# Kernel tuning notes

Measured on AMD Instinct MI355X. Metric: run time of the kernel, lower is better.

The kernel has to match this reference:

```python
import jax, jax.numpy as jnp
import numpy as np

N_NODES = 30000
N_EDGES = 480000
C = 32          # channel multiplicity of hidden irreps (32x0e + 32x1o)
L = 3           # graph_net_steps
H = 64          # radial MLP hidden width
NB = 8          # num radial basis functions
NS = 5          # num_species
R_MAX = 4.0
AVG_NEIGH = 16.0
N_PATHS = 5     # tensor-product paths per layer


def setup_inputs() -> dict:
    key = jax.random.key(0)
    ks = jax.random.split(key, 16)

    def w(k, shape, fan_in):
        return jax.random.normal(k, shape, jnp.float32) / np.sqrt(fan_in)

    return {
        "vectors": jax.random.normal(ks[0], (N_EDGES, 3), jnp.float32),
        "node_specie": jax.random.randint(ks[1], (N_NODES,), 0, NS),
        "senders": jax.random.randint(ks[2], (N_EDGES,), 0, N_NODES),
        "receivers": jax.random.randint(ks[3], (N_EDGES,), 0, N_NODES),
        "emb": jax.random.normal(ks[4], (NS, C), jnp.float32),
        "w_rad1": w(ks[5], (L, NB, H), NB),
        "w_rad2": w(ks[6], (L, H, H), H),
        "w_rad_out": w(ks[7], (L, H, N_PATHS * C), H),
        "w_lin_s": w(ks[8], (L, 2 * C, 2 * C), 2 * C),
        "w_lin_v": w(ks[9], (L, 3 * C, C), 3 * C),
        "w_sc_s": w(ks[10], (L, NS, C, 2 * C), C),
        "w_sc_v": w(ks[11], (L, NS, C, C), C),
        "w_out1": w(ks[12], (C, 16), C),
        "w_out2": w(ks[13], (16, 1), 16),
    }


def _envelope(x, p=6):
    # smooth polynomial cutoff, = 1 at x=0, = 0 (with zero derivs) at x=1
    u = (1.0 - (p + 1) * (p + 2) / 2 * x**p + p * (p + 2) * x**(p + 1)
         - p * (p + 1) / 2 * x**(p + 2))
    return jnp.where(x < 1.0, u, 0.0)


def _radial_basis(lengths):
    # bessel radial basis [E, NB] with smooth cutoff envelope
    n = jnp.arange(1, NB + 1, dtype=jnp.float32)
    x = lengths / R_MAX
    b = np.sqrt(2.0 / R_MAX) * jnp.sin(n * np.pi * x[:, None]) \
        / jnp.maximum(lengths, 1e-9)[:, None]
    return b * _envelope(x)[:, None]


def reference(vectors, node_specie, senders, receivers, emb, w_rad1, w_rad2,
              w_rad_out, w_lin_s, w_lin_v, w_sc_s, w_sc_v, w_out1, w_out2):
    vectors = vectors / R_MAX                       # as in original __call__
    lengths = jnp.linalg.norm(vectors, axis=-1)
    nhat = vectors / jnp.maximum(lengths, 1e-9)[:, None]   # unit edge vectors
    rb = _radial_basis(lengths)                     # [E, NB]

    s = emb[node_specie]                            # [N, C] scalars (0e)
    v = jnp.zeros((s.shape[0], C, 3), s.dtype)      # [N, C, 3] vectors (1o)

    for l in range(L):
        # radial MLP -> per-path, per-channel edge weights
        h = jax.nn.silu(rb @ w_rad1[l])
        h = jax.nn.silu(h @ w_rad2[l])
        wgt = (h @ w_rad_out[l]).reshape(-1, N_PATHS, C)        # [E, 5, C]

        s_u = s[senders]                                         # [E, C]
        v_u = v[senders]                                         # [E, C, 3]
        ndv = jnp.einsum('ed,ecd->ec', nhat, v_u)                # <n, v>

        # CG tensor-product message paths with spherical harmonics of n
        p0 = wgt[:, 0] * s_u                                     # 0e x Y0 -> 0e
        p1 = wgt[:, 1] * ndv                                     # 1o x Y1 -> 0e
        p2 = wgt[:, 2][:, :, None] * (s_u[:, :, None] * nhat[:, None, :])  # 0e x Y1 -> 1o
        p3 = wgt[:, 3][:, :, None] * v_u                         # 1o x Y0 -> 1o
        p4 = wgt[:, 4][:, :, None] * (nhat[:, None, :] * ndv[:, :, None] - v_u / 3.0)  # 1o x Y2 -> 1o

        agg_s = jax.ops.segment_sum(jnp.concatenate([p0, p1], 1), receivers,
                                    num_segments=N_NODES) / AVG_NEIGH      # [N, 2C]
        agg_v = jax.ops.segment_sum(jnp.concatenate([p2, p3, p4], 1), receivers,
                                    num_segments=N_NODES) / AVG_NEIGH      # [N, 3C, 3]

        sg = agg_s @ w_lin_s[l]                                  # [N, 2C]: C feats + C gates
        vn = jnp.einsum('npd,pc->ncd', agg_v, w_lin_v[l])        # [N, C, 3]
        # self-connection: per-species linear (== tp with species one-hot)
        sg = sg + jnp.einsum('nc,nck->nk', s, w_sc_s[l][node_specie])
        vn = vn + jnp.einsum('ncd,nck->nkd', v, w_sc_v[l][node_specie])

        s_new, gates = jnp.split(sg, 2, axis=1)
        s = jax.nn.silu(s_new)                                   # even activation
        v = jax.nn.silu(gates)[:, :, None] * vn                  # gated 1o

    e = (s @ w_out1) @ w_out2            # Linear '16x0e' -> Linear '0e'
    return e[:, 0]                        # per-node energy [N]
```

## Files before the change

### kernel.cpp

```cpp
#include <hip/hip_runtime.h>
#include <math.h>

#define NNODES 30000
#define NEDGES 480000
#define NC 32
#define NL 3
#define NH 64
#define NBASIS 8
#define NSPEC 5
#define INV_AVG 0.0625f

typedef _Float16 half2v __attribute__((ext_vector_type(2)));
typedef _Float16 half4v __attribute__((ext_vector_type(4)));
typedef _Float16 half8v __attribute__((ext_vector_type(8)));
typedef float    float4v __attribute__((ext_vector_type(4)));
typedef unsigned int uint32;

__device__ __forceinline__ float silu_f(float x) {
    return x / (1.f + __expf(-x));
}
__device__ __forceinline__ float rdlane(float v, int k) {
    return __uint_as_float(__builtin_amdgcn_readlane(__float_as_uint(v), k));
}


__global__ void count_kernel(const int* __restrict__ receivers, int* __restrict__ deg) {
    int e = blockIdx.x * blockDim.x + threadIdx.x;
    if (e >= NEDGES) return;
    atomicAdd(&deg[receivers[e]], 1);
}

__global__ void scan_kernel(const int* __restrict__ deg, int* __restrict__ rowstart) {
    __shared__ int lsum[256];
    __shared__ int loff[256];
    int t = threadIdx.x;
    int lo = t * 118;
    int hi = min(lo + 118, NNODES);
    int s = 0;
    for (int i = lo; i < hi; ++i) s += deg[i];
    lsum[t] = s;
    __syncthreads();
    if (t == 0) {
        int run = 0;
        for (int i = 0; i < 256; ++i) { loff[i] = run; run += lsum[i]; }
    }
    __syncthreads();
    int run = loff[t];
    for (int i = lo; i < hi; ++i) { rowstart[i] = run; run += deg[i]; }
    if (t == 0) rowstart[NNODES] = NEDGES;
}

__global__ void copy_cursor_kernel(const int* __restrict__ rowstart, int* __restrict__ cursor) {
    int i = blockIdx.x * blockDim.x + threadIdx.x;
    if (i < NNODES) cursor[i] = rowstart[i];
}

__global__ void fill_kernel(const int* __restrict__ receivers,
                            int* __restrict__ cursor, int* __restrict__ epos) {
    int e = blockIdx.x * blockDim.x + threadIdx.x;
    if (e >= NEDGES) return;
    epos[e] = atomicAdd(&cursor[receivers[e]], 1);
}

__global__ void geom_perm_kernel(const float* __restrict__ vec,
                                 const int* __restrict__ senders,
                                 const int* __restrict__ epos,
                                 float* __restrict__ nh_perm,
                                 int* __restrict__ snd_perm,
                                 float* __restrict__ rb_perm) {
    int e = blockIdx.x * blockDim.x + threadIdx.x;
    if (e >= NEDGES) return;
    float vx = vec[3*e+0] * 0.25f;
    float vy = vec[3*e+1] * 0.25f;
    float vz = vec[3*e+2] * 0.25f;
    float len = sqrtf(vx*vx + vy*vy + vz*vz);
    float inv = 1.f / fmaxf(len, 1e-9f);
    int p = epos[e];
    *(float4*)(nh_perm + (size_t)p*4) = make_float4(vx*inv, vy*inv, vz*inv, 0.f);
    snd_perm[p] = senders[e];
    float x = len * 0.25f;
    float x3 = x*x*x;
    float x6 = x3*x3;
    float x7 = x6*x;
    float x8 = x7*x;
    float env = (x < 1.f) ? (1.f - 28.f*x6 + 48.f*x7 - 21.f*x8) : 0.f;
    float scale = 0.7071067811865476f * inv * env;
    float rbv[8];
    #pragma unroll
    for (int i = 0; i < NBASIS; ++i)
        rbv[i] = scale * sinf((float)(i+1) * 3.14159265358979f * x);
    *(float4*)(rb_perm + (size_t)p*8)     = make_float4(rbv[0], rbv[1], rbv[2], rbv[3]);
    *(float4*)(rb_perm + (size_t)p*8 + 4) = make_float4(rbv[4], rbv[5], rbv[6], rbv[7]);
}

__global__ void prepw_kernel(const float* __restrict__ w1, const float* __restrict__ w2,
                             const float* __restrict__ w3,
                             float* __restrict__ w1t, _Float16* __restrict__ w2f,
                             _Float16* __restrict__ w3f) {
    int t = blockIdx.x * blockDim.x + threadIdx.x;
    if (t < NL * 64 * 8) {
        int l = t / 512, r = t % 512, k = r >> 3, b = r & 7;
        w1t[t] = w1[l * 512 + b * 64 + k];
    }
    int u = t - NL * 64 * 8;
    if (u >= 0 && u < NL * 2 * 4 * 64 * 8) {
        int e = u & 7, lane = (u >> 3) & 63, nt = (u >> 9) & 3, ks = (u >> 11) & 1, l = u >> 12;
        int k = ks * 32 + ((lane >> 4) << 3) + e;
        int col = nt * 16 + (lane & 15);
        w2f[u] = (_Float16)w2[l * 4096 + k * 64 + col];
    }
    int v = t - NL * 64 * 8 - NL * 2 * 4 * 64 * 8;
    if (v >= 0 && v < NL * 2 * 10 * 64 * 8) {
        int q = v / 5120, rem = v % 5120;
        int l = q >> 1, ks = q & 1;
        int nt = rem >> 9, lane = (rem >> 3) & 63, e = rem & 7;
        int k = ks * 32 + ((lane >> 4) << 3) + e;
        int col = nt * 16 + (lane & 15);
        w3f[v] = (_Float16)w3[l * 10240 + k * 160 + col];
    }
}

__global__ void init_kernel(const int* __restrict__ specie,
                            const float* __restrict__ emb,
                            _Float16* __restrict__ s) {
    int t = blockIdx.x * blockDim.x + threadIdx.x;
    if (t >= NNODES * NC) return;
    int n = t >> 5;
    int c = t & 31;
    s[t] = (_Float16)emb[specie[n] * NC + c];
}

__global__ __launch_bounds__(256) void mlpm_kernel(
    const float* __restrict__ rb_perm,
    const float* __restrict__ w1t,
    const _Float16* __restrict__ w2f,
    const _Float16* __restrict__ w3f,
    _Float16* __restrict__ wgt16)
{
    __shared__ float w1lds[512];
    __shared__ _Float16 tile[4][16][72];

    for (int t = threadIdx.x; t < 512; t += 256) w1lds[t] = w1t[t];
    __syncthreads();

    int lane = threadIdx.x & 63;
    int wid  = threadIdx.x >> 6;
    int c16 = lane & 15;
    int kg  = lane >> 4;
    int ibase = blockIdx.x * 64 + wid * 16;
    int g = blockIdx.x * 4 + wid;

    float4 ra4 = *(const float4*)(rb_perm + (size_t)(ibase + c16) * 8);
    float4 rb4 = *(const float4*)(rb_perm + (size_t)(ibase + c16) * 8 + 4);

    half8v a0, a1;
    #pragma unroll
    for (int e = 0; e < 8; ++e) {
        const float* wr0 = w1lds + (kg * 8 + e) * 8;
        float d0;
        d0 = ra4.x * wr0[0];
        d0 = fmaf(ra4.y, wr0[1], d0);
        d0 = fmaf(ra4.z, wr0[2], d0);
        d0 = fmaf(ra4.w, wr0[3], d0);
        d0 = fmaf(rb4.x, wr0[4], d0);
        d0 = fmaf(rb4.y, wr0[5], d0);
        d0 = fmaf(rb4.z, wr0[6], d0);
        d0 = fmaf(rb4.w, wr0[7], d0);
        a0[e] = (_Float16)silu_f(d0);
        const float* wr1 = w1lds + (32 + kg * 8 + e) * 8;
        float d1;
        d1 = ra4.x * wr1[0];
        d1 = fmaf(ra4.y, wr1[1], d1);
        d1 = fmaf(ra4.z, wr1[2], d1);
        d1 = fmaf(ra4.w, wr1[3], d1);
        d1 = fmaf(rb4.x, wr1[4], d1);
        d1 = fmaf(rb4.y, wr1[5], d1);
        d1 = fmaf(rb4.z, wr1[6], d1);
        d1 = fmaf(rb4.w, wr1[7], d1);
        a1[e] = (_Float16)silu_f(d1);
    }

    _Float16* tw = &tile[wid][0][0];
    float4v zero4 = {0.f, 0.f, 0.f, 0.f};
    #pragma unroll
    for (int nt = 0; nt < 4; ++nt) {
        half8v b0 = *(const half8v*)(w2f + (size_t)(nt) * 512 + lane * 8);
        half8v b1 = *(const half8v*)(w2f + (size_t)(4 + nt) * 512 + lane * 8);
        float4v acc = __builtin_amdgcn_mfma_f32_16x16x32_f16(a0, b0, zero4, 0, 0, 0);
        acc = __builtin_amdgcn_mfma_f32_16x16x32_f16(a1, b1, acc, 0, 0, 0);
        #pragma unroll
        for (int r = 0; r < 4; ++r)
            tw[(kg * 4 + r) * 72 + nt * 16 + c16] = (_Float16)silu_f(acc[r]);
    }

    half8v a2 = *(const half8v*)(tw + c16 * 72 + kg * 8);
    half8v a3 = *(const half8v*)(tw + c16 * 72 + 32 + kg * 8);

    _Float16* out = wgt16 + (size_t)g * 2560 + lane * 4;
    #pragma unroll
    for (int nt = 0; nt < 10; ++nt) {
        half8v b0 = *(const half8v*)(w3f + (size_t)(nt) * 512 + lane * 8);
        half8v b1 = *(const half8v*)(w3f + (size_t)(10 + nt) * 512 + lane * 8);
        float4v acc = __builtin_amdgcn_mfma_f32_16x16x32_f16(a2, b0, zero4, 0, 0, 0);
        acc = __builtin_amdgcn_mfma_f32_16x16x32_f16(a3, b1, acc, 0, 0, 0);
        half4v o;
        o[0] = (_Float16)acc[0];
        o[1] = (_Float16)acc[1];
        o[2] = (_Float16)acc[2];
        o[3] = (_Float16)acc[3];
        *(half4v*)(out + nt * 256) = o;
    }
}

__global__ __launch_bounds__(512) void gather_tp_kernel(
    const _Float16* __restrict__ wgt16,
    const float* __restrict__ nh_perm,
    const int* __restrict__ snd_perm,
    const int* __restrict__ rowstart, const int* __restrict__ deg,
    const _Float16* __restrict__ s_in, const _Float16* __restrict__ v_in,
    float* __restrict__ agg_s,
    float* __restrict__ agg_v)
{
    int lane = threadIdx.x & 63;
    int wid  = threadIdx.x >> 6;
    int n = blockIdx.x * 8 + wid;
    if (n >= NNODES) return;

    int c = lane & 31;
    int half = lane >> 5;

    int c16g = c & 15;
    int off0 = (2 * half + (c >> 4)) * 256 + c16g * 4;
    int off1 = (4 + 2 * half + (c >> 4)) * 256 + c16g * 4;
    int off2 = (8 + (c >> 4)) * 256 + c16g * 4;

    float accS = 0.f;
    float aVa0 = 0.f, aVa1 = 0.f, aVa2 = 0.f;
    float aVb0 = 0.f, aVb1 = 0.f, aVb2 = 0.f;

    int start = rowstart[n];
    int cnt   = deg[n];

    int snd_n = 0;
    float4 nh_n = make_float4(0.f, 0.f, 0.f, 0.f);
    if (cnt > 0) {
        snd_n = snd_perm[start];
        nh_n  = *(const float4*)(nh_perm + (size_t)start * 4);
    }

    for (int i = 0; i < cnt; ++i) {
        int idx = start + i;
        int snd = snd_n;
        float4 nh = nh_n;
        size_t base_e = (size_t)(idx >> 4) * 2560 + ((idx & 15) >> 2) * 64 + (idx & 3);

        float d0  = (float)wgt16[base_e + off0];
        float d1  = (float)wgt16[base_e + off1];
        float d2f = (float)wgt16[base_e + off2];

        if (i + 1 < cnt) {
            snd_n = snd_perm[idx + 1];
            nh_n  = *(const float4*)(nh_perm + (size_t)(idx + 1) * 4);
        }

        float su = (float)s_in[(size_t)snd * NC + c];
        float v0 = (float)v_in[(size_t)snd * 96 + c];
        float v1 = (float)v_in[(size_t)snd * 96 + 32 + c];
        float v2 = (float)v_in[(size_t)snd * 96 + 64 + c];
        float ndv = nh.x * v0;
        ndv = fmaf(nh.y, v1, ndv);
        ndv = fmaf(nh.z, v2, ndv);

        float sSel = half ? ndv : su;
        accS = fmaf(d0, sSel, accS);
        float scale = half ? d1 : d1 * su;
        float f0 = half ? v0 : nh.x;
        float f1 = half ? v1 : nh.y;
        float f2 = half ? v2 : nh.z;
        aVa0 = fmaf(scale, f0, aVa0);
        aVa1 = fmaf(scale, f1, aVa1);
        aVa2 = fmaf(scale, f2, aVa2);
        float m4 = half ? 0.f : d2f;
        aVb0 = fmaf(m4, fmaf(nh.x, ndv, -v0 * (1.f / 3.f)), aVb0);
        aVb1 = fmaf(m4, fmaf(nh.y, ndv, -v1 * (1.f / 3.f)), aVb1);
        aVb2 = fmaf(m4, fmaf(nh.z, ndv, -v2 * (1.f / 3.f)), aVb2);
    }

    agg_s[(size_t)n * 64 + lane] = accS;
    float* av = agg_v + (size_t)n * 288;
    if (half == 0) {
        av[c * 3 + 0] = aVa0; av[c * 3 + 1] = aVa1; av[c * 3 + 2] = aVa2;
        av[(64 + c) * 3 + 0] = aVb0; av[(64 + c) * 3 + 1] = aVb1; av[(64 + c) * 3 + 2] = aVb2;
    } else {
        av[(32 + c) * 3 + 0] = aVa0; av[(32 + c) * 3 + 1] = aVa1; av[(32 + c) * 3 + 2] = aVa2;
    }
}

__global__ __launch_bounds__(256) void node_kernel(
    const int* __restrict__ specie,
    const float* __restrict__ agg_s, const float* __restrict__ agg_v,
    const _Float16* __restrict__ s_in,  const _Float16* __restrict__ v_in,
    const float* __restrict__ wls,
    const float* __restrict__ wlv,
    const float* __restrict__ wscs,
    const float* __restrict__ wscv,
    _Float16* __restrict__ s_out, _Float16* __restrict__ v_out)
{
    __shared__ float sAV[4][288];
    __shared__ float sVO[4][96];

    int lane = threadIdx.x & 63;
    int wid  = threadIdx.x >> 6;
    int n = blockIdx.x * 4 + wid;
    if (n >= NNODES) return;
    int sp = specie[n];

    const float* av = agg_v + (size_t)n * 288;
    sAV[wid][lane]       = av[lane];
    sAV[wid][64 + lane]  = av[64 + lane];
    sAV[wid][128 + lane] = av[128 + lane];
    sAV[wid][192 + lane] = av[192 + lane];
    if (lane < 32) sAV[wid][256 + lane] = av[256 + lane];
    const _Float16* vo = v_in + (size_t)n * 96;
    if (lane < 32) {
        sVO[wid][lane]      = (float)vo[lane];
        sVO[wid][32 + lane] = (float)vo[32 + lane];
        sVO[wid][64 + lane] = (float)vo[64 + lane];
    }

    float asv = agg_s[(size_t)n * 64 + lane];
    float sv  = (float)s_in[(size_t)n * 32 + (lane & 31)];

    __syncthreads();

    float sg = 0.f;
    #pragma unroll
    for (int j = 0; j < 64; ++j)
        sg = fmaf(rdlane(asv, j), wls[j * 64 + lane], sg);
    sg *= INV_AVG;
    const float* ws = wscs + (size_t)sp * 32 * 64;
    #pragma unroll
    for (int j = 0; j < 32; ++j)
        sg = fmaf(rdlane(sv, j), ws[j * 64 + lane], sg);
    float act  = silu_f(sg);
    float gate = __shfl(act, (lane & 31) + 32);

    int c = lane & 31;
    int h = lane >> 5;
    float vn1 = 0.f, vn2 = 0.f;
    #pragma unroll
    for (int p = 0; p < 96; ++p) {
        float w = wlv[p * 32 + c];
        vn1 = fmaf(sAV[wid][3 * p + h], w, vn1);
        vn2 = fmaf(sAV[wid][3 * p + 2], w, vn2);
    }
    vn1 *= INV_AVG; vn2 *= INV_AVG;
    const float* wv = wscv + (size_t)sp * 32 * 32;
    #pragma unroll
    for (int j = 0; j < 32; ++j) {
        float w = wv[j * 32 + c];
        vn1 = fmaf(sVO[wid][h * 32 + j], w, vn1);
        vn2 = fmaf(sVO[wid][64 + j],     w, vn2);
    }

    if (lane < 32) s_out[(size_t)n * 32 + lane] = (_Float16)act;
    v_out[(size_t)n * 96 + h * 32 + c] = (_Float16)(gate * vn1);
    if (h == 0) v_out[(size_t)n * 96 + 64 + c] = (_Float16)(gate * vn2);
}

__global__ void out_kernel(const _Float16* __restrict__ s,
                           const float* __restrict__ w1,
                           const float* __restrict__ w2,
                           float* __restrict__ out) {
    int n = blockIdx.x * blockDim.x + threadIdx.x;
    if (n >= NNODES) return;
    float sv[NC];
    #pragma unroll
    for (int c = 0; c < NC; ++c) sv[c] = (float)s[(size_t)n * NC + c];
    float e = 0.f;
    #pragma unroll
    for (int j = 0; j < 16; ++j) {
        float tj = 0.f;
        #pragma unroll
        for (int c = 0; c < NC; ++c) tj += sv[c] * w1[c * 16 + j];
        e += tj * w2[j];
    }
    out[n] = e;
}

extern "C" void kernel_launch(void* const* d_in, const int* in_sizes, int n_in,
                              void* d_out, int out_size, void* d_ws, size_t ws_size,
                              hipStream_t stream) {
    const float* vectors   = (const float*)d_in[0];
    const int*   specie    = (const int*)  d_in[1];
    const int*   senders   = (const int*)  d_in[2];
    const int*   receivers = (const int*)  d_in[3];
    const float* emb       = (const float*)d_in[4];
    const float* w_rad1    = (const float*)d_in[5];
    const float* w_rad2    = (const float*)d_in[6];
    const float* w_rad_out = (const float*)d_in[7];
    const float* w_lin_s   = (const float*)d_in[8];
    const float* w_lin_v   = (const float*)d_in[9];
    const float* w_sc_s    = (const float*)d_in[10];
    const float* w_sc_v    = (const float*)d_in[11];
    const float* w_out1    = (const float*)d_in[12];
    const float* w_out2    = (const float*)d_in[13];

    char* base = (char*)d_ws;
    size_t off = 0;
    auto alloc = [&](size_t bytes) { char* q = base + off; off += (bytes + 255) & ~(size_t)255; return q; };

    float*    nh_perm  = (float*)alloc((size_t)NEDGES * 4 * 4);
    float*    rb_perm  = (float*)alloc((size_t)NEDGES * 8 * 4);
    int*      snd_perm = (int*)alloc((size_t)NEDGES * 4);
    int*      epos     = (int*)alloc((size_t)NEDGES * 4);
    _Float16* s_a      = (_Float16*)alloc((size_t)NNODES * NC * 2);
    _Float16* v_a      = (_Float16*)alloc((size_t)NNODES * NC * 3 * 2);
    _Float16* s_b      = (_Float16*)alloc((size_t)NNODES * NC * 2);
    _Float16* v_b      = (_Float16*)alloc((size_t)NNODES * NC * 3 * 2);
    float*    aggs     = (float*)alloc((size_t)NNODES * 2 * NC * 4);
    float*    aggv     = (float*)alloc((size_t)NNODES * 3 * NC * 3 * 4);
    int* deg        = (int*)alloc((size_t)NNODES * 4);
    int* rowstart   = (int*)alloc((size_t)(NNODES + 4) * 4);
    int* cursor     = (int*)alloc((size_t)NNODES * 4);
    float*    w1t      = (float*)alloc((size_t)NL * 64 * 8 * 4);
    _Float16* w2f      = (_Float16*)alloc((size_t)NL * 2 * 4 * 64 * 8 * 2);
    _Float16* w3f      = (_Float16*)alloc((size_t)NL * 2 * 10 * 64 * 8 * 2);
    _Float16* wgt16    = (_Float16*)alloc((size_t)NEDGES * 160 * 2);
    if (off > ws_size) return;

    (void)hipMemsetAsync(deg, 0, NNODES * sizeof(int), stream);
    count_kernel<<<(NEDGES + 255) / 256, 256, 0, stream>>>(receivers, deg);
    scan_kernel<<<1, 256, 0, stream>>>(deg, rowstart);
    copy_cursor_kernel<<<(NNODES + 255) / 256, 256, 0, stream>>>(rowstart, cursor);
    fill_kernel<<<(NEDGES + 255) / 256, 256, 0, stream>>>(receivers, cursor, epos);
    geom_perm_kernel<<<(NEDGES + 255) / 256, 256, 0, stream>>>(
        vectors, senders, epos, nh_perm, snd_perm, rb_perm);
    int prep_n = NL * 64 * 8 + NL * 2 * 4 * 64 * 8 + NL * 2 * 10 * 64 * 8;
    prepw_kernel<<<(prep_n + 255) / 256, 256, 0, stream>>>(
        w_rad1, w_rad2, w_rad_out, w1t, w2f, w3f);

    init_kernel<<<(NNODES * NC + 255) / 256, 256, 0, stream>>>(specie, emb, s_a);
    (void)hipMemsetAsync(v_a, 0, (size_t)NNODES * NC * 3 * 2, stream);

    _Float16* si = s_a; _Float16* vi = v_a; _Float16* so = s_b; _Float16* vo = v_b;
    for (int l = 0; l < NL; ++l) {
        mlpm_kernel<<<NEDGES / 64, 256, 0, stream>>>(
            rb_perm,
            w1t + (size_t)l * 512,
            w2f + (size_t)l * 4096,
            w3f + (size_t)l * 10240,
            wgt16);
        gather_tp_kernel<<<(NNODES + 7) / 8, 512, 0, stream>>>(
            wgt16, nh_perm, snd_perm, rowstart, deg, si, vi, aggs, aggv);
        node_kernel<<<(NNODES + 3) / 4, 256, 0, stream>>>(
            specie, aggs, aggv, si, vi,
            w_lin_s + (size_t)l * 64 * 64,
            w_lin_v + (size_t)l * 96 * 32,
            w_sc_s + (size_t)l * NSPEC * NC * 64,
            w_sc_v + (size_t)l * NSPEC * NC * NC,
            so, vo);
        _Float16* ts = si; si = so; so = ts;
        _Float16* tv = vi; vi = vo; vo = tv;
    }

    out_kernel<<<(NNODES + 255) / 256, 256, 0, stream>>>(si, w_out1, w_out2, (float*)d_out);
}
```

Baseline: 751.2 us.

## Store radial MLP weights edge-major so gather reads contiguous per-edge rows

```diff
diff --git a/kernel.cpp b/kernel.cpp
--- a/kernel.cpp
+++ b/kernel.cpp
@@ -21,6 +21,9 @@
 }
 __device__ __forceinline__ float rdlane(float v, int k) {
     return __uint_as_float(__builtin_amdgcn_readlane(__float_as_uint(v), k));
+}
+__device__ __forceinline__ half2v u2h(uint32 u) {
+    union { uint32 u; half2v h; } x; x.u = u; return x.h;
 }
 
 
@@ -138,7 +141,7 @@
     _Float16* __restrict__ wgt16)
 {
     __shared__ float w1lds[512];
-    __shared__ _Float16 tile[4][16][72];
+    __shared__ __align__(16) _Float16 lds2[4][2688];
 
     for (int t = threadIdx.x; t < 512; t += 256) w1lds[t] = w1t[t];
     __syncthreads();
@@ -180,7 +183,7 @@
         a1[e] = (_Float16)silu_f(d1);
     }
 
-    _Float16* tw = &tile[wid][0][0];
+    _Float16* tw = &lds2[wid][0];
     float4v zero4 = {0.f, 0.f, 0.f, 0.f};
     #pragma unroll
     for (int nt = 0; nt < 4; ++nt) {
@@ -196,19 +199,29 @@
     half8v a2 = *(const half8v*)(tw + c16 * 72 + kg * 8);
     half8v a3 = *(const half8v*)(tw + c16 * 72 + 32 + kg * 8);
 
-    _Float16* out = wgt16 + (size_t)g * 2560 + lane * 4;
     #pragma unroll
     for (int nt = 0; nt < 10; ++nt) {
         half8v b0 = *(const half8v*)(w3f + (size_t)(nt) * 512 + lane * 8);
         half8v b1 = *(const half8v*)(w3f + (size_t)(10 + nt) * 512 + lane * 8);
         float4v acc = __builtin_amdgcn_mfma_f32_16x16x32_f16(a2, b0, zero4, 0, 0, 0);
         acc = __builtin_amdgcn_mfma_f32_16x16x32_f16(a3, b1, acc, 0, 0, 0);
-        half4v o;
-        o[0] = (_Float16)acc[0];
-        o[1] = (_Float16)acc[1];
-        o[2] = (_Float16)acc[2];
-        o[3] = (_Float16)acc[3];
-        *(half4v*)(out + nt * 256) = o;
+        int slot;
+        if (nt < 4)      slot = nt * 32 + 2 * c16;
+        else if (nt < 8) slot = (nt - 4) * 32 + 2 * c16 + 1;
+        else             slot = 128 + (nt - 8) * 16 + c16;
+        #pragma unroll
+        for (int r = 0; r < 4; ++r)
+            tw[(kg * 4 + r) * 168 + slot] = (_Float16)acc[r];
+    }
+
+    _Float16* gout = wgt16 + (size_t)g * 2560;
+    #pragma unroll
+    for (int u = 0; u < 5; ++u) {
+        int g4 = u * 64 + lane;
+        int edge = g4 / 20;
+        int part = g4 % 20;
+        half8v vv = *(const half8v*)(tw + edge * 168 + part * 8);
+        *(half8v*)(gout + edge * 160 + part * 8) = vv;
     }
 }
 
@@ -229,11 +242,6 @@
     int c = lane & 31;
     int half = lane >> 5;
 
-    int c16g = c & 15;
-    int off0 = (2 * half + (c >> 4)) * 256 + c16g * 4;
-    int off1 = (4 + 2 * half + (c >> 4)) * 256 + c16g * 4;
-    int off2 = (8 + (c >> 4)) * 256 + c16g * 4;
-
     float accS = 0.f;
     float aVa0 = 0.f, aVa1 = 0.f, aVa2 = 0.f;
     float aVb0 = 0.f, aVb1 = 0.f, aVb2 = 0.f;
@@ -252,11 +260,12 @@
         int idx = start + i;
         int snd = snd_n;
         float4 nh = nh_n;
-        size_t base_e = (size_t)(idx >> 4) * 2560 + ((idx & 15) >> 2) * 64 + (idx & 3);
-
-        float d0  = (float)wgt16[base_e + off0];
-        float d1  = (float)wgt16[base_e + off1];
-        float d2f = (float)wgt16[base_e + off2];
+        size_t gb = (size_t)(idx >> 4) * 2560 + (size_t)(idx & 15) * 160;
+
+        half2v pr = u2h(*(const uint32*)(wgt16 + gb + lane * 2));
+        float d0  = (float)pr.x;
+        float d1  = (float)pr.y;
+        float d2f = (float)wgt16[gb + 128 + c];
 
         if (i + 1 < cnt) {
             snd_n = snd_perm[idx + 1];
```

Result: faster. 720.1 us (-4.1%).
